# Performance work log

Hardware: AMD Instinct MI355X
Metric: run time of the kernel (lower is better)

The kernel has to match this reference:

```python
import jax, jax.numpy as jnp
import numpy as np

# ---- static config (matches init_kwargs) ----
B, CIN, COUT, L = 8, 64, 64, 32768
K, STRIDE, PAD, DIL = 5, 1, 2, 1
G, DG = 4, 2                      # groups, deformable_groups_per_groups
GDG = G * DG
CD = CIN // GDG                   # channels per deformable group
DW = 7                            # depthwise kernel size of offset/mask branch
OFFSET_SCALE = 4.0
EPS = 1e-5
LOUT = (L + 2 * PAD - DIL * (K - 1) - 1) // STRIDE + 1


def setup_inputs() -> dict:
    key = jax.random.key(0)
    ks = jax.random.split(key, 8)
    s = 0.02
    f32 = jnp.float32
    return {
        "x": jax.random.normal(ks[0], (B, CIN, L), f32),
        # offset branch: depthwise conv -> per-channel groupnorm -> 1x1 conv
        "dw_off_w": (jax.random.normal(ks[1], (CIN, 1, DW), f32) * s),
        "dw_off_b": jnp.zeros((CIN,), f32),
        "gn_off_w": jnp.ones((CIN,), f32),
        "gn_off_b": jnp.zeros((CIN,), f32),
        "pw_off_w": (jax.random.normal(ks[2], (GDG * K, CIN), f32) * s),
        "pw_off_b": jnp.zeros((GDG * K,), f32),
        # attn-mask branch (same structure); final bias init to ones per repo
        "dw_m_w": (jax.random.normal(ks[3], (CIN, 1, DW), f32) * s),
        "dw_m_b": jnp.zeros((CIN,), f32),
        "gn_m_w": jnp.ones((CIN,), f32),
        "gn_m_b": jnp.zeros((CIN,), f32),
        "pw_m_w": (jax.random.normal(ks[4], (GDG * K, CIN), f32) * s),
        "pw_m_b": jnp.ones((GDG * K,), f32),
        # main conv weight (Cout, Cin/G, K) and bias, normal(0, 0.02)
        "weight": (jax.random.normal(ks[5], (COUT, CIN // G, K), f32) * s),
        "bias": (jax.random.normal(ks[6], (COUT,), f32) * s),
    }


def _dwconv(x, w, b):
    # depthwise conv1d, padding (DW-1)//2, groups = CIN
    y = jax.lax.conv_general_dilated(
        x, w, window_strides=(1,), padding=[((DW - 1) // 2, (DW - 1) // 2)],
        feature_group_count=CIN, dimension_numbers=("NCH", "OIH", "NCH"))
    return y + b[None, :, None]


def _gn_per_channel(x, g, b):
    # GroupNorm with num_groups == num_channels: normalize each channel over L
    mu = jnp.mean(x, axis=-1, keepdims=True)
    var = jnp.var(x, axis=-1, keepdims=True)
    return (x - mu) * jax.lax.rsqrt(var + EPS) * g[None, :, None] + b[None, :, None]


def _branch(x, dw_w, dw_b, gn_g, gn_b, pw_w, pw_b):
    h = _gn_per_channel(_dwconv(x, dw_w, dw_b), gn_g, gn_b)
    return jnp.einsum("oc,bcl->bol", pw_w, h) + pw_b[None, :, None]


def _deform_conv1d(x, offset, attn, weight, bias):
    # x: (B,CIN,L); offset/attn: (B,GDG*K,LOUT)
    xg = x.reshape(B, G, DG, CD, L)
    off = offset.reshape(B, G, DG, K, LOUT)
    # base sampling grid: l*stride - pad + k*dil   -> (K, LOUT)
    base = (jnp.arange(LOUT) * STRIDE - PAD)[None, :] + (jnp.arange(K) * DIL)[:, None]
    p = base.astype(x.dtype)[None, None, None] + off          # (B,G,DG,K,LOUT)
    p0 = jnp.floor(p)
    w1 = p - p0                                               # linear-interp weight
    p0i = p0.astype(jnp.int32)

    def gather(idx):
        valid = ((idx >= 0) & (idx < L)).astype(x.dtype)
        idxc = jnp.clip(idx, 0, L - 1).reshape(B, G, DG, 1, K * LOUT)
        idxc = jnp.broadcast_to(idxc, (B, G, DG, CD, K * LOUT))
        v = jnp.take_along_axis(xg, idxc, axis=-1).reshape(B, G, DG, CD, K, LOUT)
        return v * valid[:, :, :, None]

    sampled = gather(p0i) * (1.0 - w1)[:, :, :, None] + gather(p0i + 1) * w1[:, :, :, None]
    sampled = sampled * attn.reshape(B, G, DG, 1, K, LOUT)
    wg = weight.reshape(G, COUT // G, DG, CD, K)
    out = jnp.einsum("godck,bgdckl->bgol", wg, sampled).reshape(B, COUT, LOUT)
    return out + bias[None, :, None]


def reference(x, dw_off_w, dw_off_b, gn_off_w, gn_off_b, pw_off_w, pw_off_b,
              dw_m_w, dw_m_b, gn_m_w, gn_m_b, pw_m_w, pw_m_b, weight, bias):
    offset = _branch(x, dw_off_w, dw_off_b, gn_off_w, gn_off_b, pw_off_w, pw_off_b) * OFFSET_SCALE
    attn = _branch(x, dw_m_w, dw_m_b, gn_m_w, gn_m_b, pw_m_w, pw_m_b)
    # softmax modulation over the K kernel taps within each deformable group
    attn = jax.nn.softmax(attn.reshape(B, GDG, K, LOUT), axis=2).reshape(B, GDG * K, LOUT)
    return _deform_conv1d(x, offset, attn, weight, bias)
```

## Files before the change

### kernel.cpp

```cpp
#include <hip/hip_runtime.h>
#include <hip/hip_bf16.h>
#include <hip/hip_fp16.h>

typedef unsigned int   uint;
typedef unsigned short ushort;

#define NB   8
#define NC   64
#define LL   32768
#define KK   5
#define NG   4
#define NDG  2
#define NGD  8
#define NCD  8
#define NOFF 40
#define DWK  7
#define XROW (LL + 16)

typedef _Float16 f16x8 __attribute__((ext_vector_type(8)));
typedef float    f32x4 __attribute__((ext_vector_type(4)));

__device__ __forceinline__ float bf2f(ushort u) {
  union { uint u; float f; } v; v.u = ((uint)u) << 16; return v.f;
}
__device__ __forceinline__ ushort f2bf(float f) {
  union { float f; uint u; } v; v.f = f;
  uint r = (v.u + 0x7fffu + ((v.u >> 16) & 1u)) >> 16;
  return (ushort)r;
}
__device__ __forceinline__ uint pkrtz(float a, float b) {
  typedef __fp16 fp16x2n __attribute__((ext_vector_type(2)));
  fp16x2n h = __builtin_amdgcn_cvt_pkrtz(a, b);
  union { fp16x2n h; uint u; } v; v.h = h; return v.u;
}

__global__ __launch_bounds__(256) void k_prep(
    const float* __restrict__ pwA, const float* __restrict__ pwM,
    const float* __restrict__ mw,
    float* __restrict__ wtA, float* __restrict__ wtM, ushort* __restrict__ Wf)
{
  int idx = blockIdx.x * 256 + threadIdx.x;
  if (idx < 2560) {
    int c = idx / 40, o = idx % 40;
    wtA[idx] = pwA[o * NC + c];
  } else if (idx < 5120) {
    int j = idx - 2560;
    int c = j / 40, o = j % 40;
    wtM[j] = pwM[o * NC + c];
  } else if (idx < 11264) {
    int j  = idx - 5120;
    int jj = j & 7;
    int l  = (j >> 3) & 63;
    int gt = j >> 9;
    int t  = gt % 3, g = gt / 3;
    int o  = l & 15;
    int kq = t * 32 + ((l >> 4) << 3) + jj;
    float val = 0.f;
    if (kq < 80) {
      int ktap = kq >> 3, c = kq & 7;
      int d = ktap / 5, kh = ktap % 5;
      val = mw[((g * 16 + o) * 16 + d * 8 + c) * KK + kh];
    }
    Wf[j] = __half_as_ushort(__float2half(val));
  }
}

__device__ __forceinline__ void load8f(float* dst, const float* __restrict__ row,
                                       int start)
{
  if (start >= 0 && start + 8 <= LL) {
    float4 a = *(const float4*)(row + start);
    float4 b = *(const float4*)(row + start + 4);
    dst[0] = a.x; dst[1] = a.y; dst[2] = a.z; dst[3] = a.w;
    dst[4] = b.x; dst[5] = b.y; dst[6] = b.z; dst[7] = b.w;
  } else {
#pragma unroll
    for (int j = 0; j < 8; ++j) {
      int p = start + j;
      dst[j] = (p >= 0 && p < LL) ? row[p] : 0.f;
    }
  }
}

template<int WITH_XT>
__global__ __launch_bounds__(256) void k_conv(
    const float* __restrict__ x,
    const float* __restrict__ dwAw, const float* __restrict__ dwAb,
    const float* __restrict__ dwMw, const float* __restrict__ dwMb,
    ushort* __restrict__ yA, ushort* __restrict__ yM,
    ushort* __restrict__ xT, float4* __restrict__ partial)
{
  __shared__ __align__(16) ushort lx[8 * 256];
  int tid  = threadIdx.x;
  int lblk = blockIdx.x & 127;
  int gd   = (blockIdx.x >> 7) & 7;
  int b    = blockIdx.x >> 10;
  int c    = tid >> 5;
  int q    = tid & 31;
  int l0   = lblk << 8;
  int lb   = l0 + q * 8;
  int ch   = gd * 8 + c;
  const float* row = x + (size_t)(b * NC + ch) * LL;

  float v[24];
  load8f(v + 0,  row, lb - 8);
  load8f(v + 8,  row, lb);
  load8f(v + 16, row, lb + 8);

  if (WITH_XT) {
    uint4 xr;
    xr.x = pkrtz(v[8],  v[9]);
    xr.y = pkrtz(v[10], v[11]);
    xr.z = pkrtz(v[12], v[13]);
    xr.w = pkrtz(v[14], v[15]);
    *(uint4*)(lx + c * 256 + q * 8) = xr;
  }

  float wa[DWK], wm[DWK];
#pragma unroll
  for (int j = 0; j < DWK; ++j) {
    wa[j] = dwAw[ch * DWK + j];
    wm[j] = dwMw[ch * DWK + j];
  }
  float ba = dwAb[ch], bm = dwMb[ch];

  float sa = 0.f, qa = 0.f, sm = 0.f, qm = 0.f;
  uint4 pA, pM;
  ushort* ppA = (ushort*)&pA;
  ushort* ppM = (ushort*)&pM;
#pragma unroll
  for (int u = 0; u < 8; ++u) {
    float ya = ba, ym = bm;
#pragma unroll
    for (int j = 0; j < DWK; ++j) {
      float xv = v[5 + u + j];
      ya += wa[j] * xv;
      ym += wm[j] * xv;
    }
    sa += ya; qa += ya * ya;
    sm += ym; qm += ym * ym;
    ppA[u] = f2bf(ya);
    ppM[u] = f2bf(ym);
  }
  *(uint4*)(yA + (size_t)(b * NC + ch) * LL + lb) = pA;
  *(uint4*)(yM + (size_t)(b * NC + ch) * LL + lb) = pM;

#pragma unroll
  for (int m = 1; m < 32; m <<= 1) {
    sa += __shfl_xor(sa, m);
    qa += __shfl_xor(qa, m);
    sm += __shfl_xor(sm, m);
    qm += __shfl_xor(qm, m);
  }
  if (q == 0)
    partial[((size_t)(b * NC + ch) << 7) + lblk] = make_float4(sa, qa, sm, qm);

  if (WITH_XT) {
    __syncthreads();
    uint4 pk;
    pk.x = (uint)lx[0 * 256 + tid] | ((uint)lx[1 * 256 + tid] << 16);
    pk.y = (uint)lx[2 * 256 + tid] | ((uint)lx[3 * 256 + tid] << 16);
    pk.z = (uint)lx[4 * 256 + tid] | ((uint)lx[5 * 256 + tid] << 16);
    pk.w = (uint)lx[6 * 256 + tid] | ((uint)lx[7 * 256 + tid] << 16);
    size_t rowbase = (size_t)(b * NGD + gd) * (size_t)XROW;
    *(uint4*)(xT + (rowbase + 8 + (size_t)(l0 + tid)) * 8) = pk;
    if (tid < 8) {
      uint4 z = {0, 0, 0, 0};
      if (lblk == 0)   *(uint4*)(xT + (rowbase + tid) * 8) = z;
      if (lblk == 127) *(uint4*)(xT + (rowbase + 8 + LL + tid) * 8) = z;
    }
  }
}

__global__ __launch_bounds__(256) void k_fin(
    const float4* __restrict__ partial,
    const float* __restrict__ gnAw, const float* __restrict__ gnAb,
    const float* __restrict__ gnMw, const float* __restrict__ gnMb,
    const float* __restrict__ wtA, const float* __restrict__ wtM,
    const float* __restrict__ pbA, const float* __restrict__ pbM,
    float* __restrict__ wAf, float* __restrict__ wMf,
    float* __restrict__ bAf, float* __restrict__ bMf)
{
  __shared__ float4 pr[256];
  __shared__ float gA[64], cA[64], gM[64], cM[64];
  int b = blockIdx.x;
  int t = threadIdx.x;
  {
    int c = t & 63, seg = t >> 6;
    const float4* pp = partial + ((size_t)(b * NC + c) << 7);
    float4 s = make_float4(0.f, 0.f, 0.f, 0.f);
    for (int i = seg; i < 128; i += 4) {
      float4 u = pp[i];
      s.x += u.x; s.y += u.y; s.z += u.z; s.w += u.w;
    }
    pr[t] = s;
  }
  __syncthreads();
  if (t < 64) {
    float4 a0 = pr[t], a1 = pr[t + 64], a2 = pr[t + 128], a3 = pr[t + 192];
    float sx = a0.x + a1.x + a2.x + a3.x;
    float sy = a0.y + a1.y + a2.y + a3.y;
    float sz = a0.z + a1.z + a2.z + a3.z;
    float sw = a0.w + a1.w + a2.w + a3.w;
    float mua = sx / LL, vara = sy / LL - mua * mua;
    float mum = sz / LL, varm = sw / LL - mum * mum;
    float ga = gnAw[t] * rsqrtf(vara + 1e-5f);
    float gm = gnMw[t] * rsqrtf(varm + 1e-5f);
    gA[t] = ga; cA[t] = gnAb[t] - mua * ga;
    gM[t] = gm; cM[t] = gnMb[t] - mum * gm;
  }
  __syncthreads();
  for (int idx = t; idx < 2560; idx += 256) {
    int c = idx / 40;
    wAf[b * 2560 + idx] = 4.f * wtA[idx] * gA[c];
    wMf[b * 2560 + idx] = wtM[idx] * gM[c];
  }
  if (t < 40) {
    float sA = 0.f, sM = 0.f;
    for (int c = 0; c < 64; ++c) {
      sA += wtA[c * 40 + t] * cA[c];
      sM += wtM[c * 40 + t] * cM[c];
    }
    bAf[b * 40 + t] = 4.f * (pbA[t] + sA);
    bMf[b * 40 + t] = pbM[t] + sM;
  }
}

__device__ __forceinline__ void stage_matvec40(
    const ushort* __restrict__ ysrc,
    const float* __restrict__ wt,
    const float* __restrict__ pb,
    ushort* hs, int tid, float* acc)
{
#pragma unroll
  for (int i = 0; i < 8; ++i) {
    int fid = i * 256 + tid;
    int c = fid >> 5, q = fid & 31;
    ((uint4*)hs)[fid] = *(const uint4*)(ysrc + (size_t)c * LL + q * 8);
  }
  __syncthreads();
#pragma unroll
  for (int o = 0; o < NOFF; ++o) acc[o] = pb[o];
  for (int c = 0; c < NC; ++c) {
    float hv = bf2f(hs[(c << 8) + tid]);
    const float* wr = wt + c * NOFF;
#pragma unroll
    for (int o4 = 0; o4 < 10; ++o4) {
      float4 w = *(const float4*)(wr + (o4 << 2));
      acc[(o4 << 2) + 0] += w.x * hv;
      acc[(o4 << 2) + 1] += w.y * hv;
      acc[(o4 << 2) + 2] += w.z * hv;
      acc[(o4 << 2) + 3] += w.w * hv;
    }
  }
}

__global__ __launch_bounds__(256) void k_point(
    const ushort* __restrict__ yA, const ushort* __restrict__ yM,
    const float* __restrict__ wAf, const float* __restrict__ wMf,
    const float* __restrict__ bAf, const float* __restrict__ bMf,
    float* __restrict__ offs, ushort* __restrict__ attnB)
{
  __shared__ __align__(16) ushort hs[NC * 256];
  int tid = threadIdx.x;
  int b   = blockIdx.x >> 7;
  int l0  = (blockIdx.x & 127) << 8;
  int l   = l0 + tid;
  float acc[NOFF];

  stage_matvec40(yA + (size_t)b * NC * LL + l0, wAf + b * 2560, bAf + b * 40,
                 hs, tid, acc);
  {
    float* op = offs + (size_t)b * NOFF * LL + l;
#pragma unroll
    for (int o = 0; o < NOFF; ++o) op[(size_t)o * LL] = acc[o];
  }
  __syncthreads();

  stage_matvec40(yM + (size_t)b * NC * LL + l0, wMf + b * 2560, bMf + b * 40,
                 hs, tid, acc);
  {
    ushort* ap = attnB + (size_t)b * NOFF * LL + l;
#pragma unroll
    for (int g8 = 0; g8 < NGD; ++g8) {
      float mx = acc[g8 * 5];
#pragma unroll
      for (int j = 1; j < 5; ++j) mx = fmaxf(mx, acc[g8 * 5 + j]);
      float e[5]; float s = 0.f;
#pragma unroll
      for (int j = 0; j < 5; ++j) { e[j] = __expf(acc[g8 * 5 + j] - mx); s += e[j]; }
      float r = 1.f / s;
#pragma unroll
      for (int j = 0; j < 5; ++j)
        ap[(size_t)(g8 * 5 + j) * LL] =
            __half_as_ushort(__float2half(e[j] * r));
    }
  }
}

__global__ __launch_bounds__(256) void k_xpose(
    const float* __restrict__ x, ushort* __restrict__ xT)
{
  __shared__ __align__(16) float tile[8 * 256];
  int tid  = threadIdx.x;
  int lblk = blockIdx.x & 127;
  int l0   = lblk << 8;
  int gd   = (blockIdx.x >> 7) & 7;
  int b    = blockIdx.x >> 10;
  const float* src = x + (size_t)(b * NC + gd * 8) * LL + l0;
#pragma unroll
  for (int i = 0; i < 2; ++i) {
    int fid = i * 256 + tid;
    int c = fid >> 6, q = fid & 63;
    *(float4*)(tile + c * 256 + q * 4) =
        *(const float4*)(src + (size_t)c * LL + q * 4);
  }
  __syncthreads();
  uint4 pk;
  pk.x = pkrtz(tile[0 * 256 + tid], tile[1 * 256 + tid]);
  pk.y = pkrtz(tile[2 * 256 + tid], tile[3 * 256 + tid]);
  pk.z = pkrtz(tile[4 * 256 + tid], tile[5 * 256 + tid]);
  pk.w = pkrtz(tile[6 * 256 + tid], tile[7 * 256 + tid]);
  size_t rowbase = (size_t)(b * NGD + gd) * (size_t)XROW;
  *(uint4*)(xT + (rowbase + 8 + (size_t)(l0 + tid)) * 8) = pk;
  if (tid < 8) {
    uint4 z = {0, 0, 0, 0};
    if (lblk == 0)   *(uint4*)(xT + (rowbase + tid) * 8) = z;
    if (lblk == 127) *(uint4*)(xT + (rowbase + 8 + LL + tid) * 8) = z;
  }
}

__global__ __launch_bounds__(256) void k_deform(
    const ushort* __restrict__ xT, const float* __restrict__ offs,
    const ushort* __restrict__ attnH, const ushort* __restrict__ Wf,
    const float* __restrict__ bias, float* __restrict__ out)
{
  __shared__ __align__(16) char S[4 * 12288];
  int tid  = threadIdx.x;
  int wav  = tid >> 6;
  int lane = tid & 63;
  int lblk = blockIdx.x & 127;
  int g    = (blockIdx.x >> 7) & 3;
  int b    = blockIdx.x >> 9;
  int l    = (lblk << 8) + tid;

  f16x8 af[3];
#pragma unroll
  for (int t = 0; t < 3; ++t) {
    union { uint4 u; f16x8 h; } cv;
    cv.u = ((const uint4*)Wf)[(g * 3 + t) * 64 + lane];
    af[t] = cv.h;
  }

  int orow = (lane >> 4) << 2;
  float4 b4 = *(const float4*)(bias + g * 16 + orow);
  f32x4 acc[4];
#pragma unroll
  for (int nb = 0; nb < 4; ++nb) {
    acc[nb][0] = b4.x; acc[nb][1] = b4.y; acc[nb][2] = b4.z; acc[nb][3] = b4.w;
  }

  char* sb  = S + wav * 12288;
  int nbase = lane * 192;
  int msk   = (lane & 7) << 4;

  {
    f16x8 Z = {};
    *(f16x8*)(sb + ((nbase + 160) ^ msk)) = Z;
    *(f16x8*)(sb + ((nbase + 176) ^ msk)) = Z;
  }

  const float*  offp = offs  + (size_t)b * NOFF * LL + l;
  const ushort* attp = attnH + (size_t)b * NOFF * LL + l;

#pragma unroll
  for (int d = 0; d < NDG; ++d) {
    const ushort* xr = xT + (size_t)(b * NGD + g * 2 + d) * (size_t)XROW * 8;
#pragma unroll
    for (int kh = 0; kh < KK; ++kh) {
      int ch = (g * 2 + d) * KK + kh;
      float off = offp[(size_t)ch * LL];
      float at  = __half2float(__ushort_as_half(attp[(size_t)ch * LL]));
      float p   = (float)(l - 2 + kh) + off;
      p = fminf(fmaxf(p, -1.f), 32768.f);
      float p0f = floorf(p);
      float w1  = p - p0f;
      int   i0  = (int)p0f;
      float f0 = (1.f - w1) * at;
      float f1 = w1 * at;
      _Float16 a0 = (_Float16)f0;
      _Float16 a1 = (_Float16)f1;
      f16x8 F0 = {a0, a0, a0, a0, a0, a0, a0, a0};
      f16x8 F1 = {a1, a1, a1, a1, a1, a1, a1, a1};
      const ushort* q = xr + (size_t)(i0 + 8) * 8;
      f16x8 X0 = *(const f16x8*)q;
      f16x8 X1 = *(const f16x8*)(q + 8);
      f16x8 S8 = X0 * F0 + X1 * F1;
      *(f16x8*)(sb + ((nbase + (d * KK + kh) * 16) ^ msk)) = S8;
    }
  }

  int rb0 = (lane & 15) * 192 + ((lane >> 4) << 4);
#pragma unroll
  for (int nb = 0; nb < 4; ++nb) {
#pragma unroll
    for (int t = 0; t < 3; ++t) {
      f16x8 bf = *(const f16x8*)(sb + ((rb0 + nb * 3072 + t * 64) ^ msk));
      acc[nb] = __builtin_amdgcn_mfma_f32_16x16x32_f16(af[t], bf, acc[nb],
                                                       0, 0, 0);
    }
  }

  float* ob = out + (size_t)(b * NC + g * 16 + orow) * LL
              + (size_t)((lblk << 8) + (wav << 6) + (lane & 15));
#pragma unroll
  for (int nb = 0; nb < 4; ++nb) {
#pragma unroll
    for (int r = 0; r < 4; ++r)
      ob[(size_t)r * LL + (nb << 4)] = acc[nb][r];
  }
}

extern "C" void kernel_launch(void* const* d_in, const int* in_sizes, int n_in,
                              void* d_out, int out_size, void* d_ws, size_t ws_size,
                              hipStream_t stream)
{
  const float* x    = (const float*)d_in[0];
  const float* dwAw = (const float*)d_in[1];
  const float* dwAb = (const float*)d_in[2];
  const float* gnAw = (const float*)d_in[3];
  const float* gnAb = (const float*)d_in[4];
  const float* pwAw = (const float*)d_in[5];
  const float* pwAb = (const float*)d_in[6];
  const float* dwMw = (const float*)d_in[7];
  const float* dwMb = (const float*)d_in[8];
  const float* gnMw = (const float*)d_in[9];
  const float* gnMb = (const float*)d_in[10];
  const float* pwMw = (const float*)d_in[11];
  const float* pwMb = (const float*)d_in[12];
  const float* mw   = (const float*)d_in[13];
  const float* bias = (const float*)d_in[14];
  float* out = (float*)d_out;

  float* wtA = (float*)d_ws;
  float* wtM = wtA + 2560;
  ushort* Wf = (ushort*)(wtM + 2560);
  float* wAf = (float*)(Wf + 6144);
  float* wMf = wAf + 20480;
  float* bAf = wMf + 20480;
  float* bMf = bAf + 320;
  float* headEnd = bMf + 320 + 2048;
  ushort* yA = (ushort*)headEnd;
  ushort* yM = yA + (size_t)NB * NC * LL;

  const size_t xtElems  = (size_t)NB * NGD * XROW * 8;
  const size_t offElems = (size_t)NB * NOFF * LL;

  size_t needA = ((char*)(yM + (size_t)NB * NC * LL) - (char*)d_ws)
               + xtElems * 2 + offElems * 4 + offElems * 2;
  bool bigws = ws_size >= needA;

  ushort* xT;
  float* offs;
  if (bigws) {
    xT   = yM + (size_t)NB * NC * LL;
    offs = (float*)(xT + xtElems);
  } else {
    xT   = yA;
    offs = (float*)(yM + (size_t)NB * NC * LL);
  }
  ushort* attnB = (ushort*)(offs + offElems);
  float4* partial = (float4*)offs;

  hipLaunchKernelGGL(k_prep, dim3(44), dim3(256), 0, stream,
                     pwAw, pwMw, mw, wtA, wtM, Wf);
  if (bigws) {
    hipLaunchKernelGGL((k_conv<1>), dim3(NB * NGD * 128), dim3(256), 0, stream,
                       x, dwAw, dwAb, dwMw, dwMb, yA, yM, xT, partial);
  } else {
    hipLaunchKernelGGL((k_conv<0>), dim3(NB * NGD * 128), dim3(256), 0, stream,
                       x, dwAw, dwAb, dwMw, dwMb, yA, yM, (ushort*)nullptr,
                       partial);
  }
  hipLaunchKernelGGL(k_fin, dim3(NB), dim3(256), 0, stream,
                     partial, gnAw, gnAb, gnMw, gnMb, wtA, wtM, pwAb, pwMb,
                     wAf, wMf, bAf, bMf);
  hipLaunchKernelGGL(k_point, dim3(NB * (LL / 256)), dim3(256), 0, stream,
                     yA, yM, wAf, wMf, bAf, bMf, offs, attnB);
  if (!bigws) {
    hipLaunchKernelGGL(k_xpose, dim3(NB * NGD * (LL / 256)), dim3(256), 0,
                       stream, x, xT);
  }
  hipLaunchKernelGGL(k_deform, dim3(NB * NG * (LL / 256)), dim3(256), 0, stream,
                     xT, offs, attnB, Wf, bias, out);
}
```

Before: 242.4 us.

## Move pointwise offset/mask projection onto fp16 MFMA with swizzled LDS staging

```diff
diff --git a/kernel.cpp b/kernel.cpp
--- a/kernel.cpp
+++ b/kernel.cpp
@@ -20,9 +20,6 @@
 typedef _Float16 f16x8 __attribute__((ext_vector_type(8)));
 typedef float    f32x4 __attribute__((ext_vector_type(4)));
 
-__device__ __forceinline__ float bf2f(ushort u) {
-  union { uint u; float f; } v; v.u = ((uint)u) << 16; return v.f;
-}
 __device__ __forceinline__ ushort f2bf(float f) {
   union { float f; uint u; } v; v.f = f;
   uint r = (v.u + 0x7fffu + ((v.u >> 16) & 1u)) >> 16;
@@ -125,9 +122,7 @@
   float ba = dwAb[ch], bm = dwMb[ch];
 
   float sa = 0.f, qa = 0.f, sm = 0.f, qm = 0.f;
-  uint4 pA, pM;
-  ushort* ppA = (ushort*)&pA;
-  ushort* ppM = (ushort*)&pM;
+  float ya8[8], ym8[8];
 #pragma unroll
   for (int u = 0; u < 8; ++u) {
     float ya = ba, ym = bm;
@@ -139,9 +134,13 @@
     }
     sa += ya; qa += ya * ya;
     sm += ym; qm += ym * ym;
-    ppA[u] = f2bf(ya);
-    ppM[u] = f2bf(ym);
-  }
+    ya8[u] = ya; ym8[u] = ym;
+  }
+  uint4 pA, pM;
+  pA.x = pkrtz(ya8[0], ya8[1]); pA.y = pkrtz(ya8[2], ya8[3]);
+  pA.z = pkrtz(ya8[4], ya8[5]); pA.w = pkrtz(ya8[6], ya8[7]);
+  pM.x = pkrtz(ym8[0], ym8[1]); pM.y = pkrtz(ym8[2], ym8[3]);
+  pM.z = pkrtz(ym8[4], ym8[5]); pM.w = pkrtz(ym8[6], ym8[7]);
   *(uint4*)(yA + (size_t)(b * NC + ch) * LL + lb) = pA;
   *(uint4*)(yM + (size_t)(b * NC + ch) * LL + lb) = pM;
 
@@ -178,11 +177,11 @@
     const float* __restrict__ gnMw, const float* __restrict__ gnMb,
     const float* __restrict__ wtA, const float* __restrict__ wtM,
     const float* __restrict__ pbA, const float* __restrict__ pbM,
-    float* __restrict__ wAf, float* __restrict__ wMf,
-    float* __restrict__ bAf, float* __restrict__ bMf)
+    ushort* __restrict__ wF, float* __restrict__ bias48)
 {
   __shared__ float4 pr[256];
   __shared__ float gA[64], cA[64], gM[64], cM[64];
+  __shared__ float sbA[40], sbM[40];
   int b = blockIdx.x;
   int t = threadIdx.x;
   {
@@ -210,90 +209,188 @@
     gM[t] = gm; cM[t] = gnMb[t] - mum * gm;
   }
   __syncthreads();
-  for (int idx = t; idx < 2560; idx += 256) {
-    int c = idx / 40;
-    wAf[b * 2560 + idx] = 4.f * wtA[idx] * gA[c];
-    wMf[b * 2560 + idx] = wtM[idx] * gM[c];
-  }
   if (t < 40) {
     float sA = 0.f, sM = 0.f;
     for (int c = 0; c < 64; ++c) {
       sA += wtA[c * 40 + t] * cA[c];
       sM += wtM[c * 40 + t] * cM[c];
     }
-    bAf[b * 40 + t] = 4.f * (pbA[t] + sA);
-    bMf[b * 40 + t] = pbM[t] + sM;
-  }
-}
-
-__device__ __forceinline__ void stage_matvec40(
-    const ushort* __restrict__ ysrc,
-    const float* __restrict__ wt,
-    const float* __restrict__ pb,
-    ushort* hs, int tid, float* acc)
-{
-#pragma unroll
-  for (int i = 0; i < 8; ++i) {
-    int fid = i * 256 + tid;
-    int c = fid >> 5, q = fid & 31;
-    ((uint4*)hs)[fid] = *(const uint4*)(ysrc + (size_t)c * LL + q * 8);
+    sbA[t] = 4.f * (pbA[t] + sA);
+    sbM[t] = pbM[t] + sM;
+  }
+  for (int idx = t; idx < 6144; idx += 256) {
+    int br = idx >= 3072 ? 1 : 0;
+    int e  = idx - br * 3072;
+    int tt = e >> 10, ks = (e >> 9) & 1, ln = (e >> 3) & 63, j = e & 7;
+    int rr = ln & 15, h2 = rr >> 2, s = tt * 4 + (rr & 3);
+    int c  = ks * 32 + ((ln >> 4) << 3) + j;
+    float v = 0.f;
+    if (s < 10) {
+      int o = 10 * h2 + s;
+      v = br ? wtM[c * 40 + o] * gM[c] : 4.f * wtA[c * 40 + o] * gA[c];
+    }
+    wF[(size_t)b * 6144 + idx] = __half_as_ushort(__float2half(v));
   }
   __syncthreads();
-#pragma unroll
-  for (int o = 0; o < NOFF; ++o) acc[o] = pb[o];
-  for (int c = 0; c < NC; ++c) {
-    float hv = bf2f(hs[(c << 8) + tid]);
-    const float* wr = wt + c * NOFF;
-#pragma unroll
-    for (int o4 = 0; o4 < 10; ++o4) {
-      float4 w = *(const float4*)(wr + (o4 << 2));
-      acc[(o4 << 2) + 0] += w.x * hv;
-      acc[(o4 << 2) + 1] += w.y * hv;
-      acc[(o4 << 2) + 2] += w.z * hv;
-      acc[(o4 << 2) + 3] += w.w * hv;
-    }
+  if (t < 96) {
+    int br  = t >= 48 ? 1 : 0;
+    int row = t - br * 48;
+    int rr = row & 15, tt = row >> 4;
+    int h2 = rr >> 2, s = tt * 4 + (rr & 3);
+    float v = 0.f;
+    if (s < 10) { int o = 10 * h2 + s; v = br ? sbM[o] : sbA[o]; }
+    bias48[b * 96 + t] = v;
   }
 }
 
 __global__ __launch_bounds__(256) void k_point(
     const ushort* __restrict__ yA, const ushort* __restrict__ yM,
-    const float* __restrict__ wAf, const float* __restrict__ wMf,
-    const float* __restrict__ bAf, const float* __restrict__ bMf,
+    const ushort* __restrict__ wF, const float* __restrict__ bias48,
     float* __restrict__ offs, ushort* __restrict__ attnB)
 {
-  __shared__ __align__(16) ushort hs[NC * 256];
+  __shared__ __align__(16) char hsB[64 * 512];
   int tid = threadIdx.x;
   int b   = blockIdx.x >> 7;
   int l0  = (blockIdx.x & 127) << 8;
-  int l   = l0 + tid;
-  float acc[NOFF];
-
-  stage_matvec40(yA + (size_t)b * NC * LL + l0, wAf + b * 2560, bAf + b * 40,
-                 hs, tid, acc);
+  int w   = tid >> 6;
+  int ln  = tid & 63;
+  int h   = ln >> 4;
+  int col = ln & 15;
+  int msk = h << 5;
+
+  const ushort* wFb = wF + (size_t)b * 6144;
+  const float*  bb  = bias48 + b * 96;
+
   {
-    float* op = offs + (size_t)b * NOFF * LL + l;
-#pragma unroll
-    for (int o = 0; o < NOFF; ++o) op[(size_t)o * LL] = acc[o];
+    const ushort* ysrc = yA + (size_t)b * NC * LL + l0;
+#pragma unroll
+    for (int i = 0; i < 8; ++i) {
+      int fid = i * 256 + tid;
+      int c = fid >> 5, q = fid & 31;
+      *(uint4*)(hsB + c * 512 + ((q << 4) ^ (((c >> 3) & 3) << 5))) =
+          *(const uint4*)(ysrc + (size_t)c * LL + q * 8);
+    }
+    __syncthreads();
+
+    f16x8 af[3][2];
+#pragma unroll
+    for (int t = 0; t < 3; ++t)
+#pragma unroll
+      for (int ks = 0; ks < 2; ++ks) {
+        union { uint4 u; f16x8 hh; } cv;
+        cv.u = ((const uint4*)wFb)[(t * 2 + ks) * 64 + ln];
+        af[t][ks] = cv.hh;
+      }
+    f32x4 acc[3][4];
+#pragma unroll
+    for (int t = 0; t < 3; ++t) {
+      float4 bv = *(const float4*)(bb + t * 16 + h * 4);
+#pragma unroll
+      for (int nt = 0; nt < 4; ++nt) {
+        acc[t][nt][0] = bv.x; acc[t][nt][1] = bv.y;
+        acc[t][nt][2] = bv.z; acc[t][nt][3] = bv.w;
+      }
+    }
+#pragma unroll
+    for (int nt = 0; nt < 4; ++nt) {
+      int pb2 = ((((w * 4 + nt) * 16 + col) * 2) ^ msk);
+#pragma unroll
+      for (int ks = 0; ks < 2; ++ks) {
+        const char* gp = hsB + (ks * 32 + h * 8) * 512 + pb2;
+        f16x8 bf;
+#pragma unroll
+        for (int j = 0; j < 8; ++j)
+          bf[j] = *(const _Float16*)(gp + j * 512);
+#pragma unroll
+        for (int t = 0; t < 3; ++t)
+          acc[t][nt] = __builtin_amdgcn_mfma_f32_16x16x32_f16(
+              af[t][ks], bf, acc[t][nt], 0, 0, 0);
+      }
+    }
+    float* op = offs + (size_t)b * NOFF * LL + l0 + w * 64 + col;
+#pragma unroll
+    for (int t = 0; t < 3; ++t)
+#pragma unroll
+      for (int r = 0; r < 4; ++r) {
+        const int s = t * 4 + r;
+        if (s >= 10) continue;
+#pragma unroll
+        for (int nt = 0; nt < 4; ++nt)
+          op[(size_t)(10 * h + s) * LL + nt * 16] = acc[t][nt][r];
+      }
   }
   __syncthreads();
 
-  stage_matvec40(yM + (size_t)b * NC * LL + l0, wMf + b * 2560, bMf + b * 40,
-                 hs, tid, acc);
   {
-    ushort* ap = attnB + (size_t)b * NOFF * LL + l;
-#pragma unroll
-    for (int g8 = 0; g8 < NGD; ++g8) {
-      float mx = acc[g8 * 5];
-#pragma unroll
-      for (int j = 1; j < 5; ++j) mx = fmaxf(mx, acc[g8 * 5 + j]);
-      float e[5]; float s = 0.f;
-#pragma unroll
-      for (int j = 0; j < 5; ++j) { e[j] = __expf(acc[g8 * 5 + j] - mx); s += e[j]; }
-      float r = 1.f / s;
+    const ushort* ysrc = yM + (size_t)b * NC * LL + l0;
+#pragma unroll
+    for (int i = 0; i < 8; ++i) {
+      int fid = i * 256 + tid;
+      int c = fid >> 5, q = fid & 31;
+      *(uint4*)(hsB + c * 512 + ((q << 4) ^ (((c >> 3) & 3) << 5))) =
+          *(const uint4*)(ysrc + (size_t)c * LL + q * 8);
+    }
+    __syncthreads();
+
+    f16x8 af[3][2];
+#pragma unroll
+    for (int t = 0; t < 3; ++t)
+#pragma unroll
+      for (int ks = 0; ks < 2; ++ks) {
+        union { uint4 u; f16x8 hh; } cv;
+        cv.u = ((const uint4*)(wFb + 3072))[(t * 2 + ks) * 64 + ln];
+        af[t][ks] = cv.hh;
+      }
+    f32x4 acc[3][4];
+#pragma unroll
+    for (int t = 0; t < 3; ++t) {
+      float4 bv = *(const float4*)(bb + 48 + t * 16 + h * 4);
+#pragma unroll
+      for (int nt = 0; nt < 4; ++nt) {
+        acc[t][nt][0] = bv.x; acc[t][nt][1] = bv.y;
+        acc[t][nt][2] = bv.z; acc[t][nt][3] = bv.w;
+      }
+    }
+#pragma unroll
+    for (int nt = 0; nt < 4; ++nt) {
+      int pb2 = ((((w * 4 + nt) * 16 + col) * 2) ^ msk);
+#pragma unroll
+      for (int ks = 0; ks < 2; ++ks) {
+        const char* gp = hsB + (ks * 32 + h * 8) * 512 + pb2;
+        f16x8 bf;
+#pragma unroll
+        for (int j = 0; j < 8; ++j)
+          bf[j] = *(const _Float16*)(gp + j * 512);
+#pragma unroll
+        for (int t = 0; t < 3; ++t)
+          acc[t][nt] = __builtin_amdgcn_mfma_f32_16x16x32_f16(
+              af[t][ks], bf, acc[t][nt], 0, 0, 0);
+      }
+    }
+    ushort* ap = attnB + (size_t)b * NOFF * LL + l0 + w * 64 + col;
+#pragma unroll
+    for (int nt = 0; nt < 4; ++nt) {
+      float v0[5], v1[5];
+#pragma unroll
+      for (int s = 0; s < 5; ++s)  v0[s] = acc[s >> 2][nt][s & 3];
+#pragma unroll
+      for (int s = 5; s < 10; ++s) v1[s - 5] = acc[s >> 2][nt][s & 3];
+      float m0 = fmaxf(fmaxf(fmaxf(v0[0], v0[1]), fmaxf(v0[2], v0[3])), v0[4]);
+      float m1 = fmaxf(fmaxf(fmaxf(v1[0], v1[1]), fmaxf(v1[2], v1[3])), v1[4]);
+      float e0[5], e1[5], s0 = 0.f, s1 = 0.f;
+#pragma unroll
+      for (int j = 0; j < 5; ++j) { e0[j] = __expf(v0[j] - m0); s0 += e0[j]; }
+#pragma unroll
+      for (int j = 0; j < 5; ++j) { e1[j] = __expf(v1[j] - m1); s1 += e1[j]; }
+      float r0 = 1.f / s0, r1 = 1.f / s1;
 #pragma unroll
       for (int j = 0; j < 5; ++j)
-        ap[(size_t)(g8 * 5 + j) * LL] =
-            __half_as_ushort(__float2half(e[j] * r));
+        ap[(size_t)(10 * h + j) * LL + nt * 16] =
+            __half_as_ushort(__float2half(e0[j] * r0));
+#pragma unroll
+      for (int j = 0; j < 5; ++j)
+        ap[(size_t)(10 * h + 5 + j) * LL + nt * 16] =
+            __half_as_ushort(__float2half(e1[j] * r1));
     }
   }
 }
@@ -445,12 +542,9 @@
   float* wtA = (float*)d_ws;
   float* wtM = wtA + 2560;
   ushort* Wf = (ushort*)(wtM + 2560);
-  float* wAf = (float*)(Wf + 6144);
-  float* wMf = wAf + 20480;
-  float* bAf = wMf + 20480;
-  float* bMf = bAf + 320;
-  float* headEnd = bMf + 320 + 2048;
-  ushort* yA = (ushort*)headEnd;
+  ushort* wFp = Wf + 6144;
+  float* bias48 = (float*)(wFp + 49152);
+  ushort* yA = (ushort*)(bias48 + 768);
   ushort* yM = yA + (size_t)NB * NC * LL;
 
   const size_t xtElems  = (size_t)NB * NGD * XROW * 8;
@@ -484,9 +578,9 @@
   }
   hipLaunchKernelGGL(k_fin, dim3(NB), dim3(256), 0, stream,
                      partial, gnAw, gnAb, gnMw, gnMb, wtA, wtM, pwAb, pwMb,
-                     wAf, wMf, bAf, bMf);
+                     wFp, bias48);
   hipLaunchKernelGGL(k_point, dim3(NB * (LL / 256)), dim3(256), 0, stream,
-                     yA, yM, wAf, wMf, bAf, bMf, offs, attnB);
+                     yA, yM, wFp, bias48, offs, attnB);
   if (!bigws) {
     hipLaunchKernelGGL(k_xpose, dim3(NB * NGD * (LL / 256)), dim3(256), 0,
                        stream, x, xT);
```

Result: faster. 221.0 us (-8.8%).

## Fuse pointwise offset/mask projection into deform kernel using MFMA

Applied to the files above, without the earlier changes.

```diff
diff --git a/kernel.cpp b/kernel.cpp
--- a/kernel.cpp
+++ b/kernel.cpp
@@ -20,14 +20,6 @@
 typedef _Float16 f16x8 __attribute__((ext_vector_type(8)));
 typedef float    f32x4 __attribute__((ext_vector_type(4)));
 
-__device__ __forceinline__ float bf2f(ushort u) {
-  union { uint u; float f; } v; v.u = ((uint)u) << 16; return v.f;
-}
-__device__ __forceinline__ ushort f2bf(float f) {
-  union { float f; uint u; } v; v.f = f;
-  uint r = (v.u + 0x7fffu + ((v.u >> 16) & 1u)) >> 16;
-  return (ushort)r;
-}
 __device__ __forceinline__ uint pkrtz(float a, float b) {
   typedef __fp16 fp16x2n __attribute__((ext_vector_type(2)));
   fp16x2n h = __builtin_amdgcn_cvt_pkrtz(a, b);
@@ -82,7 +74,6 @@
   }
 }
 
-template<int WITH_XT>
 __global__ __launch_bounds__(256) void k_conv(
     const float* __restrict__ x,
     const float* __restrict__ dwAw, const float* __restrict__ dwAb,
@@ -107,7 +98,7 @@
   load8f(v + 8,  row, lb);
   load8f(v + 16, row, lb + 8);
 
-  if (WITH_XT) {
+  {
     uint4 xr;
     xr.x = pkrtz(v[8],  v[9]);
     xr.y = pkrtz(v[10], v[11]);
@@ -125,9 +116,7 @@
   float ba = dwAb[ch], bm = dwMb[ch];
 
   float sa = 0.f, qa = 0.f, sm = 0.f, qm = 0.f;
-  uint4 pA, pM;
-  ushort* ppA = (ushort*)&pA;
-  ushort* ppM = (ushort*)&pM;
+  float ya8[8], ym8[8];
 #pragma unroll
   for (int u = 0; u < 8; ++u) {
     float ya = ba, ym = bm;
@@ -139,9 +128,13 @@
     }
     sa += ya; qa += ya * ya;
     sm += ym; qm += ym * ym;
-    ppA[u] = f2bf(ya);
-    ppM[u] = f2bf(ym);
-  }
+    ya8[u] = ya; ym8[u] = ym;
+  }
+  uint4 pA, pM;
+  pA.x = pkrtz(ya8[0], ya8[1]); pA.y = pkrtz(ya8[2], ya8[3]);
+  pA.z = pkrtz(ya8[4], ya8[5]); pA.w = pkrtz(ya8[6], ya8[7]);
+  pM.x = pkrtz(ym8[0], ym8[1]); pM.y = pkrtz(ym8[2], ym8[3]);
+  pM.z = pkrtz(ym8[4], ym8[5]); pM.w = pkrtz(ym8[6], ym8[7]);
   *(uint4*)(yA + (size_t)(b * NC + ch) * LL + lb) = pA;
   *(uint4*)(yM + (size_t)(b * NC + ch) * LL + lb) = pM;
 
@@ -155,8 +148,8 @@
   if (q == 0)
     partial[((size_t)(b * NC + ch) << 7) + lblk] = make_float4(sa, qa, sm, qm);
 
-  if (WITH_XT) {
-    __syncthreads();
+  __syncthreads();
+  {
     uint4 pk;
     pk.x = (uint)lx[0 * 256 + tid] | ((uint)lx[1 * 256 + tid] << 16);
     pk.y = (uint)lx[2 * 256 + tid] | ((uint)lx[3 * 256 + tid] << 16);
@@ -178,11 +171,11 @@
     const float* __restrict__ gnMw, const float* __restrict__ gnMb,
     const float* __restrict__ wtA, const float* __restrict__ wtM,
     const float* __restrict__ pbA, const float* __restrict__ pbM,
-    float* __restrict__ wAf, float* __restrict__ wMf,
-    float* __restrict__ bAf, float* __restrict__ bMf)
+    ushort* __restrict__ wFp, float* __restrict__ biasPt)
 {
   __shared__ float4 pr[256];
   __shared__ float gA[64], cA[64], gM[64], cM[64];
+  __shared__ float sbA[40], sbM[40];
   int b = blockIdx.x;
   int t = threadIdx.x;
   {
@@ -210,149 +203,172 @@
     gM[t] = gm; cM[t] = gnMb[t] - mum * gm;
   }
   __syncthreads();
-  for (int idx = t; idx < 2560; idx += 256) {
-    int c = idx / 40;
-    wAf[b * 2560 + idx] = 4.f * wtA[idx] * gA[c];
-    wMf[b * 2560 + idx] = wtM[idx] * gM[c];
-  }
   if (t < 40) {
     float sA = 0.f, sM = 0.f;
     for (int c = 0; c < 64; ++c) {
       sA += wtA[c * 40 + t] * cA[c];
       sM += wtM[c * 40 + t] * cM[c];
     }
-    bAf[b * 40 + t] = 4.f * (pbA[t] + sA);
-    bMf[b * 40 + t] = pbM[t] + sM;
-  }
-}
-
-__device__ __forceinline__ void stage_matvec40(
-    const ushort* __restrict__ ysrc,
-    const float* __restrict__ wt,
-    const float* __restrict__ pb,
-    ushort* hs, int tid, float* acc)
-{
-#pragma unroll
-  for (int i = 0; i < 8; ++i) {
-    int fid = i * 256 + tid;
-    int c = fid >> 5, q = fid & 31;
-    ((uint4*)hs)[fid] = *(const uint4*)(ysrc + (size_t)c * LL + q * 8);
-  }
-  __syncthreads();
-#pragma unroll
-  for (int o = 0; o < NOFF; ++o) acc[o] = pb[o];
-  for (int c = 0; c < NC; ++c) {
-    float hv = bf2f(hs[(c << 8) + tid]);
-    const float* wr = wt + c * NOFF;
-#pragma unroll
-    for (int o4 = 0; o4 < 10; ++o4) {
-      float4 w = *(const float4*)(wr + (o4 << 2));
-      acc[(o4 << 2) + 0] += w.x * hv;
-      acc[(o4 << 2) + 1] += w.y * hv;
-      acc[(o4 << 2) + 2] += w.z * hv;
-      acc[(o4 << 2) + 3] += w.w * hv;
-    }
-  }
-}
-
-__global__ __launch_bounds__(256) void k_point(
+    sbA[t] = 4.f * (pbA[t] + sA);
+    sbM[t] = pbM[t] + sM;
+  }
+  for (int idx = t; idx < 8192; idx += 256) {
+    int br = idx >> 12;
+    int e  = idx & 4095;
+    int g  = e >> 10;
+    int ks = (e >> 9) & 1;
+    int ln = (e >> 3) & 63;
+    int j  = e & 7;
+    int rr = ln & 15;
+    int c  = ks * 32 + ((ln >> 4) << 3) + j;
+    float v = 0.f;
+    if (rr < 10) {
+      int o = 10 * g + rr;
+      v = br ? wtM[c * 40 + o] * gM[c] : 4.f * wtA[c * 40 + o] * gA[c];
+    }
+    wFp[(size_t)b * 8192 + idx] = __half_as_ushort(__float2half(v));
+  }
+  __syncthreads();
+  if (t < 128) {
+    int br = t >> 6, g = (t >> 4) & 3, m = t & 15;
+    float v = 0.f;
+    if (m < 10) v = br ? sbM[10 * g + m] : sbA[10 * g + m];
+    biasPt[b * 128 + t] = v;
+  }
+}
+
+__global__ __launch_bounds__(256) void k_pd(
     const ushort* __restrict__ yA, const ushort* __restrict__ yM,
-    const float* __restrict__ wAf, const float* __restrict__ wMf,
-    const float* __restrict__ bAf, const float* __restrict__ bMf,
-    float* __restrict__ offs, ushort* __restrict__ attnB)
-{
-  __shared__ __align__(16) ushort hs[NC * 256];
+    const ushort* __restrict__ xT,
+    const ushort* __restrict__ wFp, const float* __restrict__ biasPt,
+    const ushort* __restrict__ Wf, const float* __restrict__ bias,
+    float* __restrict__ out)
+{
+  __shared__ __align__(16) char S[4 * 12288];
   int tid = threadIdx.x;
-  int b   = blockIdx.x >> 7;
-  int l0  = (blockIdx.x & 127) << 8;
-  int l   = l0 + tid;
-  float acc[NOFF];
-
-  stage_matvec40(yA + (size_t)b * NC * LL + l0, wAf + b * 2560, bAf + b * 40,
-                 hs, tid, acc);
-  {
-    float* op = offs + (size_t)b * NOFF * LL + l;
-#pragma unroll
-    for (int o = 0; o < NOFF; ++o) op[(size_t)o * LL] = acc[o];
-  }
-  __syncthreads();
-
-  stage_matvec40(yM + (size_t)b * NC * LL + l0, wMf + b * 2560, bMf + b * 40,
-                 hs, tid, acc);
-  {
-    ushort* ap = attnB + (size_t)b * NOFF * LL + l;
-#pragma unroll
-    for (int g8 = 0; g8 < NGD; ++g8) {
-      float mx = acc[g8 * 5];
-#pragma unroll
-      for (int j = 1; j < 5; ++j) mx = fmaxf(mx, acc[g8 * 5 + j]);
-      float e[5]; float s = 0.f;
-#pragma unroll
-      for (int j = 0; j < 5; ++j) { e[j] = __expf(acc[g8 * 5 + j] - mx); s += e[j]; }
-      float r = 1.f / s;
-#pragma unroll
-      for (int j = 0; j < 5; ++j)
-        ap[(size_t)(g8 * 5 + j) * LL] =
-            __half_as_ushort(__float2half(e[j] * r));
-    }
-  }
-}
-
-__global__ __launch_bounds__(256) void k_xpose(
-    const float* __restrict__ x, ushort* __restrict__ xT)
-{
-  __shared__ __align__(16) float tile[8 * 256];
-  int tid  = threadIdx.x;
-  int lblk = blockIdx.x & 127;
-  int l0   = lblk << 8;
-  int gd   = (blockIdx.x >> 7) & 7;
-  int b    = blockIdx.x >> 10;
-  const float* src = x + (size_t)(b * NC + gd * 8) * LL + l0;
-#pragma unroll
-  for (int i = 0; i < 2; ++i) {
-    int fid = i * 256 + tid;
-    int c = fid >> 6, q = fid & 63;
-    *(float4*)(tile + c * 256 + q * 4) =
-        *(const float4*)(src + (size_t)c * LL + q * 4);
-  }
-  __syncthreads();
-  uint4 pk;
-  pk.x = pkrtz(tile[0 * 256 + tid], tile[1 * 256 + tid]);
-  pk.y = pkrtz(tile[2 * 256 + tid], tile[3 * 256 + tid]);
-  pk.z = pkrtz(tile[4 * 256 + tid], tile[5 * 256 + tid]);
-  pk.w = pkrtz(tile[6 * 256 + tid], tile[7 * 256 + tid]);
-  size_t rowbase = (size_t)(b * NGD + gd) * (size_t)XROW;
-  *(uint4*)(xT + (rowbase + 8 + (size_t)(l0 + tid)) * 8) = pk;
-  if (tid < 8) {
-    uint4 z = {0, 0, 0, 0};
-    if (lblk == 0)   *(uint4*)(xT + (rowbase + tid) * 8) = z;
-    if (lblk == 127) *(uint4*)(xT + (rowbase + 8 + LL + tid) * 8) = z;
-  }
-}
-
-__global__ __launch_bounds__(256) void k_deform(
-    const ushort* __restrict__ xT, const float* __restrict__ offs,
-    const ushort* __restrict__ attnH, const ushort* __restrict__ Wf,
-    const float* __restrict__ bias, float* __restrict__ out)
-{
-  __shared__ __align__(16) char S[4 * 12288];
-  int tid  = threadIdx.x;
-  int wav  = tid >> 6;
-  int lane = tid & 63;
-  int lblk = blockIdx.x & 127;
-  int g    = (blockIdx.x >> 7) & 3;
-  int b    = blockIdx.x >> 9;
-  int l    = (lblk << 8) + tid;
+  int w   = tid >> 6;
+  int ln  = tid & 63;
+  int h   = ln >> 4;
+  int col = ln & 15;
+  int b   = blockIdx.x >> 9;
+  int lb0 = (blockIdx.x & 511) << 6;
+
+  {
+    const ushort* srcA = yA + (size_t)b * NC * LL + lb0;
+    const ushort* srcM = yM + (size_t)b * NC * LL + lb0;
+#pragma unroll
+    for (int i = 0; i < 4; ++i) {
+      int fid = i * 256 + tid;
+      int c = fid >> 4, qc = fid & 15;
+      uint2 vA = *(const uint2*)(srcA + (size_t)c * LL + qc * 4);
+      uint2 vM = *(const uint2*)(srcM + (size_t)c * LL + qc * 4);
+      uint4 wv;
+      wv.x = __builtin_amdgcn_perm(vM.x, vA.x, 0x05040100u);
+      wv.y = __builtin_amdgcn_perm(vM.x, vA.x, 0x07060302u);
+      wv.z = __builtin_amdgcn_perm(vM.y, vA.y, 0x05040100u);
+      wv.w = __builtin_amdgcn_perm(vM.y, vA.y, 0x07060302u);
+      *(uint4*)(S + c * 256 + ((qc << 4) ^ (((c >> 3) & 3) << 6))) = wv;
+    }
+  }
+
+  const uint4* wFb = (const uint4*)(wFp + (size_t)b * 8192);
+  f16x8 afA[2], afM[2];
+#pragma unroll
+  for (int ks = 0; ks < 2; ++ks) {
+    union { uint4 u; f16x8 v; } cvA, cvM;
+    cvA.u = wFb[(w * 2 + ks) * 64 + ln];
+    cvM.u = wFb[512 + (w * 2 + ks) * 64 + ln];
+    afA[ks] = cvA.v; afM[ks] = cvM.v;
+  }
+  f32x4 accA[4], accM[4];
+  {
+    float4 bvA = *(const float4*)(biasPt + b * 128 + w * 16 + h * 4);
+    float4 bvM = *(const float4*)(biasPt + b * 128 + 64 + w * 16 + h * 4);
+#pragma unroll
+    for (int nt = 0; nt < 4; ++nt) {
+      accA[nt][0]=bvA.x; accA[nt][1]=bvA.y; accA[nt][2]=bvA.z; accA[nt][3]=bvA.w;
+      accM[nt][0]=bvM.x; accM[nt][1]=bvM.y; accM[nt][2]=bvM.z; accM[nt][3]=bvM.w;
+    }
+  }
+  __syncthreads();
+
+#pragma unroll
+  for (int nt = 0; nt < 4; ++nt) {
+#pragma unroll
+    for (int ks = 0; ks < 2; ++ks) {
+      const char* gp = S + (ks * 32 + h * 8) * 256
+                     + ((((nt * 16 + col) << 2)) ^ (h << 6));
+      uint r0 = *(const uint*)(gp + 0 * 256);
+      uint r1 = *(const uint*)(gp + 1 * 256);
+      uint r2 = *(const uint*)(gp + 2 * 256);
+      uint r3 = *(const uint*)(gp + 3 * 256);
+      uint r4 = *(const uint*)(gp + 4 * 256);
+      uint r5 = *(const uint*)(gp + 5 * 256);
+      uint r6 = *(const uint*)(gp + 6 * 256);
+      uint r7 = *(const uint*)(gp + 7 * 256);
+      union { uint u[4]; f16x8 v; } bA, bM;
+      bA.u[0] = __builtin_amdgcn_perm(r1, r0, 0x05040100u);
+      bA.u[1] = __builtin_amdgcn_perm(r3, r2, 0x05040100u);
+      bA.u[2] = __builtin_amdgcn_perm(r5, r4, 0x05040100u);
+      bA.u[3] = __builtin_amdgcn_perm(r7, r6, 0x05040100u);
+      bM.u[0] = __builtin_amdgcn_perm(r1, r0, 0x07060302u);
+      bM.u[1] = __builtin_amdgcn_perm(r3, r2, 0x07060302u);
+      bM.u[2] = __builtin_amdgcn_perm(r5, r4, 0x07060302u);
+      bM.u[3] = __builtin_amdgcn_perm(r7, r6, 0x07060302u);
+      accA[nt] = __builtin_amdgcn_mfma_f32_16x16x32_f16(afA[ks], bA.v,
+                                                        accA[nt], 0, 0, 0);
+      accM[nt] = __builtin_amdgcn_mfma_f32_16x16x32_f16(afM[ks], bM.v,
+                                                        accM[nt], 0, 0, 0);
+    }
+  }
+  __syncthreads();
+
+  char* wb = S + w * 12288;
+#pragma unroll
+  for (int r = 0; r < 4; ++r) {
+    int s = h * 4 + r;
+    if (s < 10) {
+#pragma unroll
+      for (int nt = 0; nt < 4; ++nt) {
+        int pos = nt * 16 + col;
+        *(float*)(wb + (s << 8) + (pos << 2)) = accA[nt][r];
+        *(float*)(wb + 2560 + (s << 8) + (pos << 2)) = accM[nt][r];
+      }
+    }
+  }
+  float off[10], lg[10];
+#pragma unroll
+  for (int s = 0; s < 10; ++s) {
+    off[s] = *(const float*)(wb + (s << 8) + (ln << 2));
+    lg[s]  = *(const float*)(wb + 2560 + (s << 8) + (ln << 2));
+  }
+  float at[10];
+  {
+    float m0 = fmaxf(fmaxf(fmaxf(lg[0], lg[1]), fmaxf(lg[2], lg[3])), lg[4]);
+    float m1 = fmaxf(fmaxf(fmaxf(lg[5], lg[6]), fmaxf(lg[7], lg[8])), lg[9]);
+    float e[10], s0 = 0.f, s1 = 0.f;
+#pragma unroll
+    for (int j = 0; j < 5; ++j) { e[j] = __expf(lg[j] - m0); s0 += e[j]; }
+#pragma unroll
+    for (int j = 5; j < 10; ++j) { e[j] = __expf(lg[j] - m1); s1 += e[j]; }
+    float r0 = 1.f / s0, r1 = 1.f / s1;
+#pragma unroll
+    for (int j = 0; j < 5; ++j)  at[j] = e[j] * r0;
+#pragma unroll
+    for (int j = 5; j < 10; ++j) at[j] = e[j] * r1;
+  }
+
+  int g = w;
+  int l = lb0 + ln;
 
   f16x8 af[3];
 #pragma unroll
   for (int t = 0; t < 3; ++t) {
-    union { uint4 u; f16x8 h; } cv;
-    cv.u = ((const uint4*)Wf)[(g * 3 + t) * 64 + lane];
-    af[t] = cv.h;
-  }
-
-  int orow = (lane >> 4) << 2;
+    union { uint4 u; f16x8 hh; } cv;
+    cv.u = ((const uint4*)Wf)[(g * 3 + t) * 64 + ln];
+    af[t] = cv.hh;
+  }
+  int orow = (ln >> 4) << 2;
   float4 b4 = *(const float4*)(bias + g * 16 + orow);
   f32x4 acc[4];
 #pragma unroll
@@ -360,9 +376,9 @@
     acc[nb][0] = b4.x; acc[nb][1] = b4.y; acc[nb][2] = b4.z; acc[nb][3] = b4.w;
   }
 
-  char* sb  = S + wav * 12288;
-  int nbase = lane * 192;
-  int msk   = (lane & 7) << 4;
+  char* sb  = wb;
+  int nbase = ln * 192;
+  int msk   = (ln & 7) << 4;
 
   {
     f16x8 Z = {};
@@ -370,24 +386,19 @@
     *(f16x8*)(sb + ((nbase + 176) ^ msk)) = Z;
   }
 
-  const float*  offp = offs  + (size_t)b * NOFF * LL + l;
-  const ushort* attp = attnH + (size_t)b * NOFF * LL + l;
-
 #pragma unroll
   for (int d = 0; d < NDG; ++d) {
     const ushort* xr = xT + (size_t)(b * NGD + g * 2 + d) * (size_t)XROW * 8;
 #pragma unroll
     for (int kh = 0; kh < KK; ++kh) {
-      int ch = (g * 2 + d) * KK + kh;
-      float off = offp[(size_t)ch * LL];
-      float at  = __half2float(__ushort_as_half(attp[(size_t)ch * LL]));
-      float p   = (float)(l - 2 + kh) + off;
+      int s = d * KK + kh;
+      float p = (float)(l - 2 + kh) + off[s];
       p = fminf(fmaxf(p, -1.f), 32768.f);
       float p0f = floorf(p);
       float w1  = p - p0f;
       int   i0  = (int)p0f;
-      float f0 = (1.f - w1) * at;
-      float f1 = w1 * at;
+      float f0 = (1.f - w1) * at[s];
+      float f1 = w1 * at[s];
       _Float16 a0 = (_Float16)f0;
       _Float16 a1 = (_Float16)f1;
       f16x8 F0 = {a0, a0, a0, a0, a0, a0, a0, a0};
@@ -396,11 +407,11 @@
       f16x8 X0 = *(const f16x8*)q;
       f16x8 X1 = *(const f16x8*)(q + 8);
       f16x8 S8 = X0 * F0 + X1 * F1;
-      *(f16x8*)(sb + ((nbase + (d * KK + kh) * 16) ^ msk)) = S8;
-    }
-  }
-
-  int rb0 = (lane & 15) * 192 + ((lane >> 4) << 4);
+      *(f16x8*)(sb + ((nbase + s * 16) ^ msk)) = S8;
+    }
+  }
+
+  int rb0 = (ln & 15) * 192 + ((ln >> 4) << 4);
 #pragma unroll
   for (int nb = 0; nb < 4; ++nb) {
 #pragma unroll
@@ -411,8 +422,7 @@
     }
   }
 
-  float* ob = out + (size_t)(b * NC + g * 16 + orow) * LL
-              + (size_t)((lblk << 8) + (wav << 6) + (lane & 15));
+  float* ob = out + (size_t)(b * NC + g * 16 + orow) * LL + lb0 + (ln & 15);
 #pragma unroll
   for (int nb = 0; nb < 4; ++nb) {
 #pragma unroll
@@ -445,52 +455,20 @@
   float* wtA = (float*)d_ws;
   float* wtM = wtA + 2560;
   ushort* Wf = (ushort*)(wtM + 2560);
-  float* wAf = (float*)(Wf + 6144);
-  float* wMf = wAf + 20480;
-  float* bAf = wMf + 20480;
-  float* bMf = bAf + 320;
-  float* headEnd = bMf + 320 + 2048;
-  ushort* yA = (ushort*)headEnd;
+  ushort* wFp = Wf + 6144;
+  float* biasPt = (float*)(wFp + 65536);
+  float4* partial = (float4*)(biasPt + 1024);
+  ushort* yA = (ushort*)(partial + 65536);
   ushort* yM = yA + (size_t)NB * NC * LL;
-
-  const size_t xtElems  = (size_t)NB * NGD * XROW * 8;
-  const size_t offElems = (size_t)NB * NOFF * LL;
-
-  size_t needA = ((char*)(yM + (size_t)NB * NC * LL) - (char*)d_ws)
-               + xtElems * 2 + offElems * 4 + offElems * 2;
-  bool bigws = ws_size >= needA;
-
-  ushort* xT;
-  float* offs;
-  if (bigws) {
-    xT   = yM + (size_t)NB * NC * LL;
-    offs = (float*)(xT + xtElems);
-  } else {
-    xT   = yA;
-    offs = (float*)(yM + (size_t)NB * NC * LL);
-  }
-  ushort* attnB = (ushort*)(offs + offElems);
-  float4* partial = (float4*)offs;
+  ushort* xT = yM + (size_t)NB * NC * LL;
 
   hipLaunchKernelGGL(k_prep, dim3(44), dim3(256), 0, stream,
                      pwAw, pwMw, mw, wtA, wtM, Wf);
-  if (bigws) {
-    hipLaunchKernelGGL((k_conv<1>), dim3(NB * NGD * 128), dim3(256), 0, stream,
-                       x, dwAw, dwAb, dwMw, dwMb, yA, yM, xT, partial);
-  } else {
-    hipLaunchKernelGGL((k_conv<0>), dim3(NB * NGD * 128), dim3(256), 0, stream,
-                       x, dwAw, dwAb, dwMw, dwMb, yA, yM, (ushort*)nullptr,
-                       partial);
-  }
+  hipLaunchKernelGGL(k_conv, dim3(NB * NGD * 128), dim3(256), 0, stream,
+                     x, dwAw, dwAb, dwMw, dwMb, yA, yM, xT, partial);
   hipLaunchKernelGGL(k_fin, dim3(NB), dim3(256), 0, stream,
                      partial, gnAw, gnAb, gnMw, gnMb, wtA, wtM, pwAb, pwMb,
-                     wAf, wMf, bAf, bMf);
-  hipLaunchKernelGGL(k_point, dim3(NB * (LL / 256)), dim3(256), 0, stream,
-                     yA, yM, wAf, wMf, bAf, bMf, offs, attnB);
-  if (!bigws) {
-    hipLaunchKernelGGL(k_xpose, dim3(NB * NGD * (LL / 256)), dim3(256), 0,
-                       stream, x, xT);
-  }
-  hipLaunchKernelGGL(k_deform, dim3(NB * NG * (LL / 256)), dim3(256), 0, stream,
-                     xT, offs, attnB, Wf, bias, out);
-}
+                     wFp, biasPt);
+  hipLaunchKernelGGL(k_pd, dim3(NB * 512), dim3(256), 0, stream,
+                     yA, yM, xT, wFp, biasPt, Wf, bias, out);
+}
```

Measured after the change: 197.5 us. -18.6%, faster.
